# Optimization experiments

Measured on AMD Instinct MI355X. Metric: run time of the kernel, lower is better.

Reference implementation:

```python
import jax, jax.numpy as jnp
import numpy as np

DM = 1024
H = 16
DEPTH = DM // H


def setup_inputs() -> dict:
    key = jax.random.key(0)
    ks = jax.random.split(key, 12)
    B, S = 2, 2048
    s_in = 1.0 / np.sqrt(DM)
    inp = {
        "Q": jax.random.normal(ks[0], (B, S, DM), dtype=jnp.float32),
        "K": jax.random.normal(ks[1], (B, S, DM), dtype=jnp.float32),
        "V": jax.random.normal(ks[2], (B, S, DM), dtype=jnp.float32),
        "mask": jnp.zeros((B, 1, 1, S), dtype=jnp.float32),
        "Wq": jax.random.normal(ks[3], (DM, DM), dtype=jnp.float32) * s_in,
        "bq": jnp.zeros((DM,), dtype=jnp.float32),
        "Wk": jax.random.normal(ks[4], (DM, DM), dtype=jnp.float32) * s_in,
        "bk": jnp.zeros((DM,), dtype=jnp.float32),
        "Wv": jax.random.normal(ks[5], (DM, DM), dtype=jnp.float32) * s_in,
        "bv": jnp.zeros((DM,), dtype=jnp.float32),
        "Wo": jax.random.normal(ks[6], (DM, DM), dtype=jnp.float32) * s_in,
        "bo": jnp.zeros((DM,), dtype=jnp.float32),
    }
    return inp


def reference(Q, K, V, mask, Wq, bq, Wk, bk, Wv, bv, Wo, bo):
    B, S, _ = Q.shape
    # QKV projections, then split into heads: (B, h, S, depth)
    def split_heads(x):
        return x.reshape(B, S, H, DEPTH).transpose(0, 2, 1, 3)

    q = split_heads(Q @ Wq + bq)
    k = split_heads(K @ Wk + bk)
    v = split_heads(V @ Wv + bv)

    # scaled dot-product attention
    scale = 1.0 / jnp.sqrt(jnp.asarray(DEPTH, dtype=q.dtype))
    scores = jnp.einsum("bhqd,bhkd->bhqk", q, k) * scale
    scores = scores + mask * -1e9  # additive mask (zeros => no-op)
    weights = jax.nn.softmax(scores, axis=-1)  # (B, h, Sq, Sk)
    ctx = jnp.einsum("bhqk,bhkd->bhqd", weights, v)

    # merge heads and output projection
    concat = ctx.transpose(0, 2, 1, 3).reshape(B, S, DM)
    output = concat @ Wo + bo
    return output, weights
```

## Files before the change

### kernel.cpp

```cpp
#include <hip/hip_runtime.h>
#include <hip/hip_bf16.h>

#define S_LEN 2048
#define DMODEL 1024
#define NH 16
#define DHEAD 64
#define M_TOT 4096

typedef __attribute__((ext_vector_type(8))) short bf16x8;
typedef __attribute__((ext_vector_type(4))) float f32x4;

__device__ __forceinline__ short f2bf(float x) {
  __hip_bfloat16 h = __float2bfloat16(x);
  short s; __builtin_memcpy(&s, &h, 2); return s;
}
__device__ __forceinline__ float bf2f(short s) {
  __hip_bfloat16 h; __builtin_memcpy(&h, &s, 2);
  return __bfloat162float(h);
}

__device__ __forceinline__ void async16(const short* g, short* l) {
  __builtin_amdgcn_global_load_lds(
      (const __attribute__((address_space(1))) unsigned int*)g,
      (__attribute__((address_space(3))) unsigned int*)l, 16, 0, 0);
}

__device__ __forceinline__ void stage_tile(const short* __restrict__ src, int row0,
                                           int k0, short* lds, int t) {
  const int r = t >> 2, c = (t & 3) << 3;
  async16(src + (size_t)(row0 + r) * DMODEL + k0 + c, lds + t * 8);
  async16(src + (size_t)(row0 + 64 + r) * DMODEL + k0 + c, lds + 2048 + t * 8);
}

__global__ void split_cvt(const float* __restrict__ src, short* __restrict__ hi,
                          short* __restrict__ lo, int n4) {
  int i = blockIdx.x * blockDim.x + threadIdx.x;
  if (i >= n4) return;
  float4 x = reinterpret_cast<const float4*>(src)[i];
  short4 h, l;
  h.x = f2bf(x.x); h.y = f2bf(x.y); h.z = f2bf(x.z); h.w = f2bf(x.w);
  l.x = f2bf(x.x - bf2f(h.x)); l.y = f2bf(x.y - bf2f(h.y));
  l.z = f2bf(x.z - bf2f(h.z)); l.w = f2bf(x.w - bf2f(h.w));
  reinterpret_cast<short4*>(hi)[i] = h;
  reinterpret_cast<short4*>(lo)[i] = l;
}

__global__ void transpose_split_w(const float* __restrict__ W,
                                  short* __restrict__ hiT, short* __restrict__ loT) {
  __shared__ float t[32][33];
  int tx = threadIdx.x;
  int kb = blockIdx.y * 32;
  int nb = blockIdx.x * 32;
  for (int ty = threadIdx.y; ty < 32; ty += 8)
    t[ty][tx] = W[(size_t)(kb + ty) * DMODEL + nb + tx];
  __syncthreads();
  for (int ty = threadIdx.y; ty < 32; ty += 8) {
    float x = t[tx][ty];
    short hv = f2bf(x);
    hiT[(size_t)(nb + ty) * DMODEL + kb + tx] = hv;
    loT[(size_t)(nb + ty) * DMODEL + kb + tx] = f2bf(x - bf2f(hv));
  }
}

__launch_bounds__(256)
__global__ void proj_gemm(
    const short* __restrict__ qa_hi, const short* __restrict__ qa_lo,
    const short* __restrict__ ka_hi, const short* __restrict__ ka_lo,
    const short* __restrict__ va_hi, const short* __restrict__ va_lo,
    const short* __restrict__ wq_hiT, const short* __restrict__ wq_loT,
    const short* __restrict__ wk_hiT, const short* __restrict__ wk_loT,
    const short* __restrict__ wv_hiT, const short* __restrict__ wv_loT,
    const float* __restrict__ bq, const float* __restrict__ bk,
    const float* __restrict__ bv,
    short* __restrict__ qh, short* __restrict__ kh, short* __restrict__ vT) {
  const int which = blockIdx.z;
  const short* Ahi = (which == 0) ? qa_hi : (which == 1) ? ka_hi : va_hi;
  const short* Alo = (which == 0) ? qa_lo : (which == 1) ? ka_lo : va_lo;
  const short* Bhi = (which == 0) ? wq_hiT : (which == 1) ? wk_hiT : wv_hiT;
  const short* Blo = (which == 0) ? wq_loT : (which == 1) ? wk_loT : wv_loT;
  const float* bias = (which == 0) ? bq : (which == 1) ? bk : bv;

  const int m0 = blockIdx.y * 128, n0 = blockIdx.x * 128;
  const int t = threadIdx.x;
  const int lane = t & 63, wave = t >> 6;
  const int wm = (wave >> 1) * 64, wn = (wave & 1) * 64;
  const int lm = lane & 15, quad = lane >> 4;

  __shared__ short sAh[128 * 32], sAl[128 * 32];
  __shared__ short sBh[128 * 32], sBl[128 * 32];

  f32x4 acc[4][4];
#pragma unroll
  for (int i = 0; i < 4; i++)
#pragma unroll
    for (int j = 0; j < 4; j++) acc[i][j] = (f32x4){0.f, 0.f, 0.f, 0.f};

  for (int k0 = 0; k0 < DMODEL; k0 += 32) {
    stage_tile(Ahi, m0, k0, sAh, t);
    stage_tile(Alo, m0, k0, sAl, t);
    stage_tile(Bhi, n0, k0, sBh, t);
    stage_tile(Blo, n0, k0, sBl, t);
    __syncthreads();

    bf16x8 ah[4], al[4], bh[4], bl[4];
#pragma unroll
    for (int i = 0; i < 4; i++) {
      ah[i] = *reinterpret_cast<const bf16x8*>(sAh + (wm + i * 16 + lm) * 32 + quad * 8);
      al[i] = *reinterpret_cast<const bf16x8*>(sAl + (wm + i * 16 + lm) * 32 + quad * 8);
    }
#pragma unroll
    for (int j = 0; j < 4; j++) {
      bh[j] = *reinterpret_cast<const bf16x8*>(sBh + (wn + j * 16 + lm) * 32 + quad * 8);
      bl[j] = *reinterpret_cast<const bf16x8*>(sBl + (wn + j * 16 + lm) * 32 + quad * 8);
    }
#pragma unroll
    for (int i = 0; i < 4; i++)
#pragma unroll
      for (int j = 0; j < 4; j++) {
        acc[i][j] = __builtin_amdgcn_mfma_f32_16x16x32_bf16(ah[i], bh[j], acc[i][j], 0, 0, 0);
        acc[i][j] = __builtin_amdgcn_mfma_f32_16x16x32_bf16(ah[i], bl[j], acc[i][j], 0, 0, 0);
        acc[i][j] = __builtin_amdgcn_mfma_f32_16x16x32_bf16(al[i], bh[j], acc[i][j], 0, 0, 0);
      }
    __syncthreads();
  }

#pragma unroll
  for (int j = 0; j < 4; j++) {
    const int col = n0 + wn + j * 16 + lm;
    const float bb = bias[col];
    const int hh = col >> 6, dd = col & 63;
#pragma unroll
    for (int i = 0; i < 4; i++) {
#pragma unroll
      for (int r = 0; r < 4; r++) {
        const int row = m0 + wm + i * 16 + quad * 4 + r;
        const int bidx = row >> 11, ss = row & 2047;
        const float v = acc[i][j][r] + bb;
        if (which < 2) {
          short* dst = (which == 0) ? qh : kh;
          dst[(((size_t)(bidx * NH + hh) * S_LEN) + ss) * DHEAD + dd] = f2bf(v);
        } else {
          vT[(((size_t)(bidx * NH + hh) * DHEAD) + dd) * S_LEN + ss] = f2bf(v);
        }
      }
    }
  }
}

__launch_bounds__(256)
__global__ void score_exp(const short* __restrict__ qh, const short* __restrict__ kh,
                          const float* __restrict__ mask,
                          float* __restrict__ wout, float* __restrict__ rsum) {
  const int bh = blockIdx.z;
  const int m0 = blockIdx.y * 128, n0 = blockIdx.x * 128;
  const int lane = threadIdx.x & 63, wave = threadIdx.x >> 6;
  const int wm = (wave >> 1) * 64, wn = (wave & 1) * 64;
  const int lm = lane & 15, quad = lane >> 4;
  const short* qb = qh + (size_t)bh * S_LEN * DHEAD;
  const short* kb = kh + (size_t)bh * S_LEN * DHEAD;

  f32x4 acc[4][4];
#pragma unroll
  for (int i = 0; i < 4; i++)
#pragma unroll
    for (int j = 0; j < 4; j++) acc[i][j] = (f32x4){0.f, 0.f, 0.f, 0.f};

#pragma unroll
  for (int k0 = 0; k0 < DHEAD; k0 += 32) {
    bf16x8 a[4], b[4];
#pragma unroll
    for (int i = 0; i < 4; i++)
      a[i] = *reinterpret_cast<const bf16x8*>(qb + (size_t)(m0 + wm + i * 16 + lm) * DHEAD + k0 + quad * 8);
#pragma unroll
    for (int j = 0; j < 4; j++)
      b[j] = *reinterpret_cast<const bf16x8*>(kb + (size_t)(n0 + wn + j * 16 + lm) * DHEAD + k0 + quad * 8);
#pragma unroll
    for (int i = 0; i < 4; i++)
#pragma unroll
      for (int j = 0; j < 4; j++)
        acc[i][j] = __builtin_amdgcn_mfma_f32_16x16x32_bf16(a[i], b[j], acc[i][j], 0, 0, 0);
  }

  const int b_ = bh >> 4;
  float msk[4];
#pragma unroll
  for (int j = 0; j < 4; j++)
    msk[j] = mask[(size_t)b_ * S_LEN + n0 + wn + j * 16 + lm] * -1e9f;

  float* wb = wout + (size_t)bh * S_LEN * S_LEN;
  float se[4][4];
#pragma unroll
  for (int i = 0; i < 4; i++)
#pragma unroll
    for (int r = 0; r < 4; r++) se[i][r] = 0.f;

#pragma unroll
  for (int i = 0; i < 4; i++) {
#pragma unroll
    for (int j = 0; j < 4; j++) {
#pragma unroll
      for (int r = 0; r < 4; r++) {
        const int row = m0 + wm + i * 16 + quad * 4 + r;
        const int col = n0 + wn + j * 16 + lm;
        float e = __expf(acc[i][j][r] * 0.125f + msk[j]);
        wb[(size_t)row * S_LEN + col] = e;
        se[i][r] += e;
      }
    }
  }
#pragma unroll
  for (int i = 0; i < 4; i++) {
#pragma unroll
    for (int r = 0; r < 4; r++) {
      float v = se[i][r];
      v += __shfl_xor(v, 1); v += __shfl_xor(v, 2);
      v += __shfl_xor(v, 4); v += __shfl_xor(v, 8);
      if (lm == 0)
        atomicAdd(&rsum[(size_t)bh * S_LEN + m0 + wm + i * 16 + quad * 4 + r], v);
    }
  }
}

__launch_bounds__(256)
__global__ void pv_norm(float* __restrict__ wio, const short* __restrict__ vT,
                        const float* __restrict__ rsum, short* __restrict__ ctxB) {
  const int bh = blockIdx.y;
  const int mt = blockIdx.x;
  const int lane = threadIdx.x & 63, wave = threadIdx.x >> 6;
  const int lm = lane & 15, quad = lane >> 4;
  const int mbase = mt * 128 + wave * 32;
  float* wb = wio + (size_t)bh * S_LEN * S_LEN;
  const short* vb = vT + (size_t)bh * DHEAD * S_LEN;

  float rinv[2];
#pragma unroll
  for (int i = 0; i < 2; i++)
    rinv[i] = 1.0f / rsum[(size_t)bh * S_LEN + mbase + i * 16 + lm];

  f32x4 acc[2][4];
#pragma unroll
  for (int i = 0; i < 2; i++)
#pragma unroll
    for (int j = 0; j < 4; j++) acc[i][j] = (f32x4){0.f, 0.f, 0.f, 0.f};

  for (int k0 = 0; k0 < S_LEN; k0 += 32) {
    bf16x8 a[2];
#pragma unroll
    for (int i = 0; i < 2; i++) {
      float4* p = reinterpret_cast<float4*>(wb + (size_t)(mbase + i * 16 + lm) * S_LEN + k0 + quad * 8);
      float4 x0 = p[0], x1 = p[1];
      x0.x *= rinv[i]; x0.y *= rinv[i]; x0.z *= rinv[i]; x0.w *= rinv[i];
      x1.x *= rinv[i]; x1.y *= rinv[i]; x1.z *= rinv[i]; x1.w *= rinv[i];
      p[0] = x0; p[1] = x1;
      bf16x8 av;
      av[0] = f2bf(x0.x); av[1] = f2bf(x0.y); av[2] = f2bf(x0.z); av[3] = f2bf(x0.w);
      av[4] = f2bf(x1.x); av[5] = f2bf(x1.y); av[6] = f2bf(x1.z); av[7] = f2bf(x1.w);
      a[i] = av;
    }
    bf16x8 b[4];
#pragma unroll
    for (int j = 0; j < 4; j++)
      b[j] = *reinterpret_cast<const bf16x8*>(vb + (size_t)(j * 16 + lm) * S_LEN + k0 + quad * 8);
#pragma unroll
    for (int i = 0; i < 2; i++)
#pragma unroll
      for (int j = 0; j < 4; j++)
        acc[i][j] = __builtin_amdgcn_mfma_f32_16x16x32_bf16(a[i], b[j], acc[i][j], 0, 0, 0);
  }

  const int b_ = bh >> 4, h = bh & 15;
#pragma unroll
  for (int i = 0; i < 2; i++)
#pragma unroll
    for (int j = 0; j < 4; j++)
#pragma unroll
      for (int r = 0; r < 4; r++) {
        const int ss = mbase + i * 16 + quad * 4 + r;
        const int dd = j * 16 + lm;
        ctxB[((size_t)(b_ * S_LEN + ss)) * DMODEL + h * DHEAD + dd] = f2bf(acc[i][j][r]);
      }
}

__launch_bounds__(256)
__global__ void out_gemm(const short* __restrict__ ctxB, const short* __restrict__ woT,
                         const float* __restrict__ bo, float* __restrict__ out) {
  const int m0 = blockIdx.y * 128, n0 = blockIdx.x * 128;
  const int t = threadIdx.x;
  const int lane = t & 63, wave = t >> 6;
  const int wm = (wave >> 1) * 64, wn = (wave & 1) * 64;
  const int lm = lane & 15, quad = lane >> 4;

  __shared__ short sA[128 * 32], sB[128 * 32];

  f32x4 acc[4][4];
#pragma unroll
  for (int i = 0; i < 4; i++)
#pragma unroll
    for (int j = 0; j < 4; j++) acc[i][j] = (f32x4){0.f, 0.f, 0.f, 0.f};

  for (int k0 = 0; k0 < DMODEL; k0 += 32) {
    stage_tile(ctxB, m0, k0, sA, t);
    stage_tile(woT, n0, k0, sB, t);
    __syncthreads();

    bf16x8 a[4], b[4];
#pragma unroll
    for (int i = 0; i < 4; i++)
      a[i] = *reinterpret_cast<const bf16x8*>(sA + (wm + i * 16 + lm) * 32 + quad * 8);
#pragma unroll
    for (int j = 0; j < 4; j++)
      b[j] = *reinterpret_cast<const bf16x8*>(sB + (wn + j * 16 + lm) * 32 + quad * 8);
#pragma unroll
    for (int i = 0; i < 4; i++)
#pragma unroll
      for (int j = 0; j < 4; j++)
        acc[i][j] = __builtin_amdgcn_mfma_f32_16x16x32_bf16(a[i], b[j], acc[i][j], 0, 0, 0);
    __syncthreads();
  }

#pragma unroll
  for (int j = 0; j < 4; j++) {
    const int col = n0 + wn + j * 16 + lm;
    const float bb = bo[col];
#pragma unroll
    for (int i = 0; i < 4; i++)
#pragma unroll
      for (int r = 0; r < 4; r++) {
        const int row = m0 + wm + i * 16 + quad * 4 + r;
        out[(size_t)row * DMODEL + col] = acc[i][j][r] + bb;
      }
  }
}

extern "C" void kernel_launch(void* const* d_in, const int* in_sizes, int n_in,
                              void* d_out, int out_size, void* d_ws, size_t ws_size,
                              hipStream_t stream) {
  const float* Q = (const float*)d_in[0];
  const float* K = (const float*)d_in[1];
  const float* V = (const float*)d_in[2];
  const float* mask = (const float*)d_in[3];
  const float* Wq = (const float*)d_in[4];
  const float* bq = (const float*)d_in[5];
  const float* Wk = (const float*)d_in[6];
  const float* bk = (const float*)d_in[7];
  const float* Wv = (const float*)d_in[8];
  const float* bv = (const float*)d_in[9];
  const float* Wo = (const float*)d_in[10];
  const float* bo = (const float*)d_in[11];

  float* out0 = (float*)d_out;
  float* weights = (float*)d_out + (size_t)M_TOT * DMODEL;

  char* w = (char*)d_ws;
  const size_t MB = 1ull << 20;
  short* qh = (short*)(w + 0 * MB);
  short* kh = (short*)(w + 8 * MB);
  short* vT = (short*)(w + 16 * MB);
  short* ctxB = (short*)(w + 24 * MB);
  float* rsum = (float*)(w + 32 * MB);
  short* wq_hiT = (short*)(w + 33 * MB);
  short* wq_loT = (short*)(w + 35 * MB);
  short* wk_hiT = (short*)(w + 37 * MB);
  short* wk_loT = (short*)(w + 39 * MB);
  short* wv_hiT = (short*)(w + 41 * MB);
  short* wv_loT = (short*)(w + 43 * MB);
  short* wo_hiT = (short*)(w + 45 * MB);
  short* wo_loT = (short*)(w + 47 * MB);
  short* qa_hi = (short*)(w + 49 * MB);
  short* qa_lo = (short*)(w + 57 * MB);
  short* ka_hi = (short*)(w + 65 * MB);
  short* ka_lo = (short*)(w + 73 * MB);
  short* va_hi = (short*)(w + 81 * MB);
  short* va_lo = (short*)(w + 89 * MB);

  const int n4 = M_TOT * DMODEL / 4;
  split_cvt<<<dim3(n4 / 256), 256, 0, stream>>>(Q, qa_hi, qa_lo, n4);
  split_cvt<<<dim3(n4 / 256), 256, 0, stream>>>(K, ka_hi, ka_lo, n4);
  split_cvt<<<dim3(n4 / 256), 256, 0, stream>>>(V, va_hi, va_lo, n4);
  transpose_split_w<<<dim3(32, 32), dim3(32, 8), 0, stream>>>(Wq, wq_hiT, wq_loT);
  transpose_split_w<<<dim3(32, 32), dim3(32, 8), 0, stream>>>(Wk, wk_hiT, wk_loT);
  transpose_split_w<<<dim3(32, 32), dim3(32, 8), 0, stream>>>(Wv, wv_hiT, wv_loT);
  transpose_split_w<<<dim3(32, 32), dim3(32, 8), 0, stream>>>(Wo, wo_hiT, wo_loT);
  hipMemsetAsync(rsum, 0, 65536 * sizeof(float), stream);

  proj_gemm<<<dim3(8, 32, 3), 256, 0, stream>>>(
      qa_hi, qa_lo, ka_hi, ka_lo, va_hi, va_lo,
      wq_hiT, wq_loT, wk_hiT, wk_loT, wv_hiT, wv_loT,
      bq, bk, bv, qh, kh, vT);
  score_exp<<<dim3(16, 16, 32), 256, 0, stream>>>(qh, kh, mask, weights, rsum);
  pv_norm<<<dim3(16, 32), 256, 0, stream>>>(weights, vT, rsum, ctxB);
  out_gemm<<<dim3(8, 32), 256, 0, stream>>>(ctxB, wo_hiT, bo, out0);
}
```

Measured before the change: 1.179 ms.

## Compute softmax row sums first, then fuse normalized weights write with PV

```diff
diff --git a/kernel.cpp b/kernel.cpp
--- a/kernel.cpp
+++ b/kernel.cpp
@@ -148,136 +148,184 @@
 }
 
 __launch_bounds__(256)
-__global__ void score_exp(const short* __restrict__ qh, const short* __restrict__ kh,
-                          const float* __restrict__ mask,
-                          float* __restrict__ wout, float* __restrict__ rsum) {
-  const int bh = blockIdx.z;
-  const int m0 = blockIdx.y * 128, n0 = blockIdx.x * 128;
+__global__ void row_sums(const short* __restrict__ qh, const short* __restrict__ kh,
+                         const float* __restrict__ mask, float* __restrict__ rsum) {
+  const int bh = blockIdx.y;
+  const int m0 = blockIdx.x * 128;
   const int lane = threadIdx.x & 63, wave = threadIdx.x >> 6;
-  const int wm = (wave >> 1) * 64, wn = (wave & 1) * 64;
+  const int lm = lane & 15, quad = lane >> 4;
+  const int wrow = m0 + wave * 32;
+  const short* qb = qh + (size_t)bh * S_LEN * DHEAD;
+  const short* kb = kh + (size_t)bh * S_LEN * DHEAD;
+  const float* mrow = mask + (size_t)(bh >> 4) * S_LEN;
+
+  bf16x8 aq[2][2];
+#pragma unroll
+  for (int i = 0; i < 2; i++)
+#pragma unroll
+    for (int k = 0; k < 2; k++)
+      aq[i][k] = *reinterpret_cast<const bf16x8*>(
+          qb + (size_t)(wrow + i * 16 + lm) * DHEAD + k * 32 + quad * 8);
+
+  float rs[2][4];
+#pragma unroll
+  for (int i = 0; i < 2; i++)
+#pragma unroll
+    for (int r = 0; r < 4; r++) rs[i][r] = 0.f;
+
+  for (int n = 0; n < S_LEN; n += 64) {
+    bf16x8 bk[4][2];
+#pragma unroll
+    for (int j = 0; j < 4; j++)
+#pragma unroll
+      for (int k = 0; k < 2; k++)
+        bk[j][k] = *reinterpret_cast<const bf16x8*>(
+            kb + (size_t)(n + j * 16 + lm) * DHEAD + k * 32 + quad * 8);
+    f32x4 acc[2][4];
+#pragma unroll
+    for (int i = 0; i < 2; i++)
+#pragma unroll
+      for (int j = 0; j < 4; j++) acc[i][j] = (f32x4){0.f, 0.f, 0.f, 0.f};
+#pragma unroll
+    for (int k = 0; k < 2; k++)
+#pragma unroll
+      for (int i = 0; i < 2; i++)
+#pragma unroll
+        for (int j = 0; j < 4; j++)
+          acc[i][j] = __builtin_amdgcn_mfma_f32_16x16x32_bf16(aq[i][k], bk[j][k], acc[i][j], 0, 0, 0);
+
+    float msk[4];
+#pragma unroll
+    for (int j = 0; j < 4; j++) msk[j] = mrow[n + j * 16 + lm] * -1e9f;
+#pragma unroll
+    for (int i = 0; i < 2; i++)
+#pragma unroll
+      for (int j = 0; j < 4; j++)
+#pragma unroll
+        for (int r = 0; r < 4; r++)
+          rs[i][r] += __expf(acc[i][j][r] * 0.125f + msk[j]);
+  }
+#pragma unroll
+  for (int i = 0; i < 2; i++)
+#pragma unroll
+    for (int r = 0; r < 4; r++) {
+      float v = rs[i][r];
+      v += __shfl_xor(v, 1); v += __shfl_xor(v, 2);
+      v += __shfl_xor(v, 4); v += __shfl_xor(v, 8);
+      if (lm == 0)
+        rsum[(size_t)bh * S_LEN + wrow + i * 16 + quad * 4 + r] = v;
+    }
+}
+
+__launch_bounds__(256)
+__global__ void attn_fused(const short* __restrict__ qh, const short* __restrict__ kh,
+                           const short* __restrict__ vT, const float* __restrict__ mask,
+                           const float* __restrict__ rsum,
+                           float* __restrict__ wout, short* __restrict__ ctxB) {
+  const int bh = blockIdx.y;
+  const int m0 = blockIdx.x * 128;
+  const int lane = threadIdx.x & 63, wave = threadIdx.x >> 6;
+  const int wm = (wave >> 1) * 64, wn = (wave & 1) * 64, wn2 = (wave & 1) * 32;
   const int lm = lane & 15, quad = lane >> 4;
   const short* qb = qh + (size_t)bh * S_LEN * DHEAD;
   const short* kb = kh + (size_t)bh * S_LEN * DHEAD;
-
-  f32x4 acc[4][4];
-#pragma unroll
-  for (int i = 0; i < 4; i++)
-#pragma unroll
-    for (int j = 0; j < 4; j++) acc[i][j] = (f32x4){0.f, 0.f, 0.f, 0.f};
-
-#pragma unroll
-  for (int k0 = 0; k0 < DHEAD; k0 += 32) {
-    bf16x8 a[4], b[4];
-#pragma unroll
-    for (int i = 0; i < 4; i++)
-      a[i] = *reinterpret_cast<const bf16x8*>(qb + (size_t)(m0 + wm + i * 16 + lm) * DHEAD + k0 + quad * 8);
+  const short* vb = vT + (size_t)bh * DHEAD * S_LEN;
+  float* wb = wout + (size_t)bh * S_LEN * S_LEN;
+  const float* mrow = mask + (size_t)(bh >> 4) * S_LEN;
+
+  bf16x8 aq[4][2];
+#pragma unroll
+  for (int i = 0; i < 4; i++)
+#pragma unroll
+    for (int k = 0; k < 2; k++)
+      aq[i][k] = *reinterpret_cast<const bf16x8*>(
+          qb + (size_t)(m0 + wm + i * 16 + lm) * DHEAD + k * 32 + quad * 8);
+
+  float rinv[4][4];
+#pragma unroll
+  for (int i = 0; i < 4; i++)
+#pragma unroll
+    for (int r = 0; r < 4; r++)
+      rinv[i][r] = 1.0f / rsum[(size_t)bh * S_LEN + m0 + wm + i * 16 + quad * 4 + r];
+
+  f32x4 ctx[4][2];
+#pragma unroll
+  for (int i = 0; i < 4; i++)
+#pragma unroll
+    for (int j = 0; j < 2; j++) ctx[i][j] = (f32x4){0.f, 0.f, 0.f, 0.f};
+
+  for (int c = 0; c < S_LEN; c += 128) {
+    bf16x8 bk[4][2];
 #pragma unroll
     for (int j = 0; j < 4; j++)
-      b[j] = *reinterpret_cast<const bf16x8*>(kb + (size_t)(n0 + wn + j * 16 + lm) * DHEAD + k0 + quad * 8);
+#pragma unroll
+      for (int k = 0; k < 2; k++)
+        bk[j][k] = *reinterpret_cast<const bf16x8*>(
+            kb + (size_t)(c + wn + j * 16 + lm) * DHEAD + k * 32 + quad * 8);
+    f32x4 s[4][4];
+#pragma unroll
+    for (int i = 0; i < 4; i++)
+#pragma unroll
+      for (int j = 0; j < 4; j++) s[i][j] = (f32x4){0.f, 0.f, 0.f, 0.f};
+#pragma unroll
+    for (int k = 0; k < 2; k++)
+#pragma unroll
+      for (int i = 0; i < 4; i++)
+#pragma unroll
+        for (int j = 0; j < 4; j++)
+          s[i][j] = __builtin_amdgcn_mfma_f32_16x16x32_bf16(aq[i][k], bk[j][k], s[i][j], 0, 0, 0);
+
+    float msk[4];
+#pragma unroll
+    for (int j = 0; j < 4; j++) msk[j] = mrow[c + wn + j * 16 + lm] * -1e9f;
 #pragma unroll
     for (int i = 0; i < 4; i++)
 #pragma unroll
       for (int j = 0; j < 4; j++)
-        acc[i][j] = __builtin_amdgcn_mfma_f32_16x16x32_bf16(a[i], b[j], acc[i][j], 0, 0, 0);
-  }
-
-  const int b_ = bh >> 4;
-  float msk[4];
-#pragma unroll
-  for (int j = 0; j < 4; j++)
-    msk[j] = mask[(size_t)b_ * S_LEN + n0 + wn + j * 16 + lm] * -1e9f;
-
-  float* wb = wout + (size_t)bh * S_LEN * S_LEN;
-  float se[4][4];
-#pragma unroll
-  for (int i = 0; i < 4; i++)
-#pragma unroll
-    for (int r = 0; r < 4; r++) se[i][r] = 0.f;
-
-#pragma unroll
-  for (int i = 0; i < 4; i++) {
-#pragma unroll
-    for (int j = 0; j < 4; j++) {
+#pragma unroll
+        for (int r = 0; r < 4; r++) {
+          const int row = m0 + wm + i * 16 + quad * 4 + r;
+          float e = __expf(s[i][j][r] * 0.125f + msk[j]) * rinv[i][r];
+          wb[(size_t)row * S_LEN + c + wn + j * 16 + lm] = e;
+        }
+    __syncthreads();
+
+#pragma unroll
+    for (int kk = 0; kk < 128; kk += 32) {
+      bf16x8 ap[4];
+#pragma unroll
+      for (int i = 0; i < 4; i++) {
+        const float4* p = reinterpret_cast<const float4*>(
+            wb + (size_t)(m0 + wm + i * 16 + lm) * S_LEN + c + kk + quad * 8);
+        float4 x0 = p[0], x1 = p[1];
+        bf16x8 av;
+        av[0] = f2bf(x0.x); av[1] = f2bf(x0.y); av[2] = f2bf(x0.z); av[3] = f2bf(x0.w);
+        av[4] = f2bf(x1.x); av[5] = f2bf(x1.y); av[6] = f2bf(x1.z); av[7] = f2bf(x1.w);
+        ap[i] = av;
+      }
+      bf16x8 bv[2];
+#pragma unroll
+      for (int j = 0; j < 2; j++)
+        bv[j] = *reinterpret_cast<const bf16x8*>(
+            vb + (size_t)(wn2 + j * 16 + lm) * S_LEN + c + kk + quad * 8);
+#pragma unroll
+      for (int i = 0; i < 4; i++)
+#pragma unroll
+        for (int j = 0; j < 2; j++)
+          ctx[i][j] = __builtin_amdgcn_mfma_f32_16x16x32_bf16(ap[i], bv[j], ctx[i][j], 0, 0, 0);
+    }
+  }
+
+  const int b_ = bh >> 4, h = bh & 15;
+#pragma unroll
+  for (int i = 0; i < 4; i++)
+#pragma unroll
+    for (int j = 0; j < 2; j++)
 #pragma unroll
       for (int r = 0; r < 4; r++) {
-        const int row = m0 + wm + i * 16 + quad * 4 + r;
-        const int col = n0 + wn + j * 16 + lm;
-        float e = __expf(acc[i][j][r] * 0.125f + msk[j]);
-        wb[(size_t)row * S_LEN + col] = e;
-        se[i][r] += e;
-      }
-    }
-  }
-#pragma unroll
-  for (int i = 0; i < 4; i++) {
-#pragma unroll
-    for (int r = 0; r < 4; r++) {
-      float v = se[i][r];
-      v += __shfl_xor(v, 1); v += __shfl_xor(v, 2);
-      v += __shfl_xor(v, 4); v += __shfl_xor(v, 8);
-      if (lm == 0)
-        atomicAdd(&rsum[(size_t)bh * S_LEN + m0 + wm + i * 16 + quad * 4 + r], v);
-    }
-  }
-}
-
-__launch_bounds__(256)
-__global__ void pv_norm(float* __restrict__ wio, const short* __restrict__ vT,
-                        const float* __restrict__ rsum, short* __restrict__ ctxB) {
-  const int bh = blockIdx.y;
-  const int mt = blockIdx.x;
-  const int lane = threadIdx.x & 63, wave = threadIdx.x >> 6;
-  const int lm = lane & 15, quad = lane >> 4;
-  const int mbase = mt * 128 + wave * 32;
-  float* wb = wio + (size_t)bh * S_LEN * S_LEN;
-  const short* vb = vT + (size_t)bh * DHEAD * S_LEN;
-
-  float rinv[2];
-#pragma unroll
-  for (int i = 0; i < 2; i++)
-    rinv[i] = 1.0f / rsum[(size_t)bh * S_LEN + mbase + i * 16 + lm];
-
-  f32x4 acc[2][4];
-#pragma unroll
-  for (int i = 0; i < 2; i++)
-#pragma unroll
-    for (int j = 0; j < 4; j++) acc[i][j] = (f32x4){0.f, 0.f, 0.f, 0.f};
-
-  for (int k0 = 0; k0 < S_LEN; k0 += 32) {
-    bf16x8 a[2];
-#pragma unroll
-    for (int i = 0; i < 2; i++) {
-      float4* p = reinterpret_cast<float4*>(wb + (size_t)(mbase + i * 16 + lm) * S_LEN + k0 + quad * 8);
-      float4 x0 = p[0], x1 = p[1];
-      x0.x *= rinv[i]; x0.y *= rinv[i]; x0.z *= rinv[i]; x0.w *= rinv[i];
-      x1.x *= rinv[i]; x1.y *= rinv[i]; x1.z *= rinv[i]; x1.w *= rinv[i];
-      p[0] = x0; p[1] = x1;
-      bf16x8 av;
-      av[0] = f2bf(x0.x); av[1] = f2bf(x0.y); av[2] = f2bf(x0.z); av[3] = f2bf(x0.w);
-      av[4] = f2bf(x1.x); av[5] = f2bf(x1.y); av[6] = f2bf(x1.z); av[7] = f2bf(x1.w);
-      a[i] = av;
-    }
-    bf16x8 b[4];
-#pragma unroll
-    for (int j = 0; j < 4; j++)
-      b[j] = *reinterpret_cast<const bf16x8*>(vb + (size_t)(j * 16 + lm) * S_LEN + k0 + quad * 8);
-#pragma unroll
-    for (int i = 0; i < 2; i++)
-#pragma unroll
-      for (int j = 0; j < 4; j++)
-        acc[i][j] = __builtin_amdgcn_mfma_f32_16x16x32_bf16(a[i], b[j], acc[i][j], 0, 0, 0);
-  }
-
-  const int b_ = bh >> 4, h = bh & 15;
-#pragma unroll
-  for (int i = 0; i < 2; i++)
-#pragma unroll
-    for (int j = 0; j < 4; j++)
-#pragma unroll
-      for (int r = 0; r < 4; r++) {
-        const int ss = mbase + i * 16 + quad * 4 + r;
-        const int dd = j * 16 + lm;
-        ctxB[((size_t)(b_ * S_LEN + ss)) * DMODEL + h * DHEAD + dd] = f2bf(acc[i][j][r]);
+        const int ss = m0 + wm + i * 16 + quad * 4 + r;
+        const int dd = wn2 + j * 16 + lm;
+        ctxB[((size_t)(b_ * S_LEN + ss)) * DMODEL + h * DHEAD + dd] = f2bf(ctx[i][j][r]);
       }
 }
 
@@ -381,13 +429,12 @@
   transpose_split_w<<<dim3(32, 32), dim3(32, 8), 0, stream>>>(Wk, wk_hiT, wk_loT);
   transpose_split_w<<<dim3(32, 32), dim3(32, 8), 0, stream>>>(Wv, wv_hiT, wv_loT);
   transpose_split_w<<<dim3(32, 32), dim3(32, 8), 0, stream>>>(Wo, wo_hiT, wo_loT);
-  hipMemsetAsync(rsum, 0, 65536 * sizeof(float), stream);
 
   proj_gemm<<<dim3(8, 32, 3), 256, 0, stream>>>(
       qa_hi, qa_lo, ka_hi, ka_lo, va_hi, va_lo,
       wq_hiT, wq_loT, wk_hiT, wk_loT, wv_hiT, wv_loT,
       bq, bk, bv, qh, kh, vT);
-  score_exp<<<dim3(16, 16, 32), 256, 0, stream>>>(qh, kh, mask, weights, rsum);
-  pv_norm<<<dim3(16, 32), 256, 0, stream>>>(weights, vT, rsum, ctxB);
+  row_sums<<<dim3(16, 32), 256, 0, stream>>>(qh, kh, mask, rsum);
+  attn_fused<<<dim3(16, 32), 256, 0, stream>>>(qh, kh, vT, mask, rsum, weights, ctxB);
   out_gemm<<<dim3(8, 32), 256, 0, stream>>>(ctxB, wo_hiT, bo, out0);
 }
```

After: 1.056 ms. 1.12x faster.
